# Kernel optimization log

Hardware: AMD Instinct MI355X
Metric: run time of the kernel (lower is better)

## Reference

```python
import jax, jax.numpy as jnp
import numpy as np

NUM_HEADS = 16
EMBED_DIM = 1024
SEQ_LEN = 2048
BATCH = 2


def setup_inputs() -> dict:
    key = jax.random.key(0)
    ks = jax.random.split(key, 7)
    E = EMBED_DIM
    scale = 1.0 / np.sqrt(E)
    return {
        "query": jax.random.normal(ks[0], (SEQ_LEN, BATCH, E), jnp.float32),
        "key": jax.random.normal(ks[1], (SEQ_LEN, BATCH, E), jnp.float32),
        "value": jax.random.normal(ks[2], (SEQ_LEN, BATCH, E), jnp.float32),
        "in_proj_weight": jax.random.normal(ks[3], (3 * E, E), jnp.float32) * scale,
        "in_proj_bias": jnp.zeros((3 * E,), jnp.float32),
        "out_proj_weight": jax.random.normal(ks[4], (E, E), jnp.float32) * scale,
        "out_proj_bias": jnp.zeros((E,), jnp.float32),
    }


def reference(query, key, value, in_proj_weight, in_proj_bias, out_proj_weight, out_proj_bias):
    T, B, E = query.shape
    H = NUM_HEADS
    d = E // H
    scaling = float(d) ** -0.5
    # in-projections: rows [0:E) -> q, [E:2E) -> k, [2E:3E) -> v
    q = query @ in_proj_weight[:E].T + in_proj_bias[:E]
    k = key @ in_proj_weight[E:2 * E].T + in_proj_bias[E:2 * E]
    v = value @ in_proj_weight[2 * E:].T + in_proj_bias[2 * E:]
    q = q * scaling
    # (T, B, E) -> (B*H, T, d)
    q = q.reshape(T, B * H, d).transpose(1, 0, 2)
    k = k.reshape(T, B * H, d).transpose(1, 0, 2)
    v = v.reshape(T, B * H, d).transpose(1, 0, 2)
    S = k.shape[1]
    scores = jnp.einsum('ntd,nsd->nts', q, k)  # (B*H, T, S)
    attn = jax.nn.softmax(scores, axis=-1)
    out = jnp.einsum('nts,nsd->ntd', attn, v)  # (B*H, T, d)
    out = out.transpose(1, 0, 2).reshape(T, B, E)
    out = out @ out_proj_weight.T + out_proj_bias
    attn_avg = attn.reshape(B, H, T, S).sum(axis=1) / H
    return out, attn_avg
```

## Files before the change

kernel.cpp:

```cpp
#include <hip/hip_runtime.h>
#include <math.h>

#define T_LEN 2048
#define BATCH 2
#define EMB 1024
#define NHEAD 16
#define HDIM 64
#define BH (BATCH*NHEAD)
#define MROWS (T_LEN*BATCH)
#define QSCALE (0.125f * 1.4426950408889634f)
#define HEADBUF ((size_t)BH*T_LEN*HDIM)

typedef __attribute__((ext_vector_type(8))) short bf16x8;
typedef __attribute__((ext_vector_type(4))) float f32x4;

#define MFMA16(a,b,c) __builtin_amdgcn_mfma_f32_16x16x32_bf16(a,b,c,0,0,0)

__device__ __forceinline__ short f2bf(float f) {
    union { float f; unsigned u; } v; v.f = f;
    unsigned r = (v.u + 0x7FFFu + ((v.u >> 16) & 1u)) >> 16;
    return (short)(unsigned short)r;
}
__device__ __forceinline__ float bf2f(short s) {
    union { unsigned u; float f; } v; v.u = ((unsigned)(unsigned short)s) << 16;
    return v.f;
}
__device__ __forceinline__ unsigned cvtpk(float a, float b) {
    unsigned r;
    asm("v_cvt_pk_bf16_f32 %0, %1, %2" : "=v"(r) : "v"(a), "v"(b));
    return r;
}
__device__ __forceinline__ void gload16(const void* g, void* l) {
    __builtin_amdgcn_global_load_lds(
        (const __attribute__((address_space(1))) unsigned*)g,
        (__attribute__((address_space(3))) unsigned*)l, 16, 0, 0);
}

__global__ __launch_bounds__(256) void tobf16_kernel(
    const float* __restrict__ q, const float* __restrict__ k,
    const float* __restrict__ v, const float* __restrict__ w,
    const float* __restrict__ wo, short* __restrict__ out)
{
    size_t i8 = ((size_t)blockIdx.x * 256 + threadIdx.x) * 8;
    const float* src; size_t off;
    if (i8 < 12582912) {
        int sel = (int)(i8 >> 22);
        src = (sel == 0) ? q : (sel == 1) ? k : v;
        off = i8 & 4194303;
    } else if (i8 < 15728640) {
        src = w;  off = i8 - 12582912;
    } else {
        src = wo; off = i8 - 15728640;
    }
    float4 f0 = *(const float4*)(src + off);
    float4 f1 = *(const float4*)(src + off + 4);
    bf16x8 o;
    o[0]=f2bf(f0.x); o[1]=f2bf(f0.y); o[2]=f2bf(f0.z); o[3]=f2bf(f0.w);
    o[4]=f2bf(f1.x); o[5]=f2bf(f1.y); o[6]=f2bf(f1.z); o[7]=f2bf(f1.w);
    *(bf16x8*)(out + i8) = o;
}

__global__ __launch_bounds__(256) void inproj_gemm(
    const short* __restrict__ Xq, const short* __restrict__ Xk,
    const short* __restrict__ Xv, const short* __restrict__ Wb,
    const float* __restrict__ bias,
    short* __restrict__ qbuf, short* __restrict__ kbuf, short* __restrict__ vbufT)
{
    const int mBase = blockIdx.x * 128;
    const int nBase = blockIdx.y * 128;
    const int which = nBase >> 10;
    const short* __restrict__ X = (which == 0) ? Xq : (which == 1) ? Xk : Xv;

    __shared__ short Ast[2][128][32];
    __shared__ short Bst[2][128][32];

    const int tid  = threadIdx.x;
    const int lane = tid & 63;
    const int w    = tid >> 6;
    const int wr   = w >> 1, wc = w & 1;
    const int lr   = lane & 15, lg = lane >> 4;

    const int srow = lane >> 2;
    const int schk = (lane & 3) ^ ((lane >> 3) & 3);
    const int fchk = (lg ^ ((lr >> 1) & 3)) * 16;

    f32x4 acc[4][4] = {};

    #pragma unroll
    for (int j = 0; j < 2; ++j) {
        int r = j * 64 + w * 16 + srow;
        gload16(X  + (size_t)(mBase + r) * EMB + schk * 8,
                (char*)Ast[0] + j * 4096 + w * 1024);
        gload16(Wb + (size_t)(nBase + r) * EMB + schk * 8,
                (char*)Bst[0] + j * 4096 + w * 1024);
    }
    __syncthreads();

    int cur = 0;
    for (int kb = 0; kb < EMB; kb += 32) {
        if (kb + 32 < EMB) {
            #pragma unroll
            for (int j = 0; j < 2; ++j) {
                int r = j * 64 + w * 16 + srow;
                gload16(X  + (size_t)(mBase + r) * EMB + kb + 32 + schk * 8,
                        (char*)Ast[cur ^ 1] + j * 4096 + w * 1024);
                gload16(Wb + (size_t)(nBase + r) * EMB + kb + 32 + schk * 8,
                        (char*)Bst[cur ^ 1] + j * 4096 + w * 1024);
            }
        }
        bf16x8 af[4], bfr[4];
        #pragma unroll
        for (int rg = 0; rg < 4; ++rg)
            af[rg] = *(const bf16x8*)((char*)Ast[cur] + (wr * 64 + rg * 16 + lr) * 64 + fchk);
        #pragma unroll
        for (int cg = 0; cg < 4; ++cg)
            bfr[cg] = *(const bf16x8*)((char*)Bst[cur] + (wc * 64 + cg * 16 + lr) * 64 + fchk);
        #pragma unroll
        for (int rg = 0; rg < 4; ++rg)
            #pragma unroll
            for (int cg = 0; cg < 4; ++cg)
                acc[rg][cg] = MFMA16(af[rg], bfr[cg], acc[rg][cg]);
        __syncthreads();
        cur ^= 1;
    }

    #pragma unroll
    for (int rg = 0; rg < 4; ++rg) {
        #pragma unroll
        for (int cg = 0; cg < 4; ++cg) {
            int n  = nBase + wc * 64 + cg * 16 + lr;
            int e  = n & 1023;
            int h  = e >> 6, dd = e & 63;
            float bs = bias[n];
            #pragma unroll
            for (int ri = 0; ri < 4; ++ri) {
                int m = mBase + wr * 64 + rg * 16 + lg * 4 + ri;
                int t = m >> 1, b = m & 1;
                float val = acc[rg][cg][ri] + bs;
                short bfv;
                if (which == 0) { bfv = f2bf(val * QSCALE);
                    qbuf[((size_t)(b * NHEAD + h) * T_LEN + t) * HDIM + dd] = bfv; }
                else if (which == 1) { bfv = f2bf(val);
                    kbuf[((size_t)(b * NHEAD + h) * T_LEN + t) * HDIM + dd] = bfv; }
                else {
                    bfv = f2bf(val);
                    int s5 = t & 31;
                    int kk = ((s5 >> 2) & 3) * 8 + ((s5 >> 4) << 2) + (s5 & 3);
                    int tt = (t & ~31) | kk;
                    vbufT[((size_t)(b * NHEAD + h) * HDIM + dd) * T_LEN + tt] = bfv;
                }
            }
        }
    }
}

__global__ __launch_bounds__(256) void flash_kernel(
    const short* __restrict__ qb, const short* __restrict__ kbuf,
    const short* __restrict__ vbufT, short* __restrict__ h1,
    float* __restrict__ mlws)
{
    const int qt = blockIdx.x;
    const int hb = blockIdx.y;

    __shared__ short Kst[2][64][64];
    __shared__ short Vst[2][64][64];

    const int tid  = threadIdx.x;
    const int lane = tid & 63;
    const int w    = tid >> 6;
    const int lr   = lane & 15, lg = lane >> 4;

    bf16x8 qa0, qa1;
    {
        const short* qsrc = qb + ((size_t)hb * T_LEN + qt * 64 + w * 16 + lr) * HDIM;
        qa0 = *(const bf16x8*)(qsrc + lg * 8);
        qa1 = *(const bf16x8*)(qsrc + 32 + lg * 8);
    }

    const short* kbase = kbuf  + (size_t)hb * T_LEN * HDIM;
    const short* vbase = vbufT + (size_t)hb * HDIM * T_LEN;

    const int krow = lane >> 3;
    const int kc16 = (lane & 7) ^ krow;
    const int rb0 = ((0 + lg) ^ (lr & 7)) * 16;
    const int rb1 = ((4 + lg) ^ (lr & 7)) * 16;

    float l_r = 0.f;
    f32x4 o_acc[4] = {};

    for (int st = 0; st < T_LEN / 128; ++st) {
        __syncthreads();
        #pragma unroll
        for (int it = 0; it < 2; ++it) {
            int r = (w * 2 + it) * 8 + krow;
            #pragma unroll
            for (int sh = 0; sh < 2; ++sh) {
                gload16(kbase + (size_t)(st * 128 + sh * 64 + r) * HDIM + kc16 * 8,
                        (char*)Kst[sh] + (w * 2 + it) * 1024);
                gload16(vbase + (size_t)r * T_LEN + st * 128 + sh * 64 + kc16 * 8,
                        (char*)Vst[sh] + (w * 2 + it) * 1024);
            }
        }
        __syncthreads();

        #pragma unroll
        for (int sh = 0; sh < 2; ++sh) {
            f32x4 sc[4] = {};
            #pragma unroll
            for (int sg = 0; sg < 4; ++sg) {
                const char* krowp = (const char*)Kst[sh] + (sg * 16 + lr) * 128;
                bf16x8 kf0 = *(const bf16x8*)(krowp + rb0);
                bf16x8 kf1 = *(const bf16x8*)(krowp + rb1);
                sc[sg] = MFMA16(kf0, qa0, sc[sg]);
                sc[sg] = MFMA16(kf1, qa1, sc[sg]);
            }

            float p[4][4];
            #pragma unroll
            for (int sg = 0; sg < 4; ++sg)
                #pragma unroll
                for (int ri = 0; ri < 4; ++ri) {
                    p[sg][ri] = exp2f(sc[sg][ri]);
                    l_r += p[sg][ri];
                }

            #pragma unroll
            for (int ks = 0; ks < 2; ++ks) {
                union { unsigned u[4]; bf16x8 v; } pau;
                pau.u[0] = cvtpk(p[ks * 2][0],     p[ks * 2][1]);
                pau.u[1] = cvtpk(p[ks * 2][2],     p[ks * 2][3]);
                pau.u[2] = cvtpk(p[ks * 2 + 1][0], p[ks * 2 + 1][1]);
                pau.u[3] = cvtpk(p[ks * 2 + 1][2], p[ks * 2 + 1][3]);
                #pragma unroll
                for (int dsub = 0; dsub < 4; ++dsub) {
                    const char* vrowp = (const char*)Vst[sh] + (dsub * 16 + lr) * 128;
                    bf16x8 vf = *(const bf16x8*)(vrowp + (ks ? rb1 : rb0));
                    o_acc[dsub] = MFMA16(pau.v, vf, o_acc[dsub]);
                }
            }
        }
    }

    float lsum = l_r;
    lsum += __shfl_xor(lsum, 16);
    lsum += __shfl_xor(lsum, 32);
    float inv = 1.0f / lsum;
    float invq[4];
    #pragma unroll
    for (int ri = 0; ri < 4; ++ri) invq[ri] = __shfl(inv, lg * 20 + ri);
    #pragma unroll
    for (int ri = 0; ri < 4; ++ri) {
        int row = qt * 64 + w * 16 + lg * 4 + ri;
        #pragma unroll
        for (int dsub = 0; dsub < 4; ++dsub) {
            float x = o_acc[dsub][ri] * invq[ri];
            h1[((size_t)hb * T_LEN + row) * HDIM + dsub * 16 + lr] = f2bf(x);
        }
    }
    if (lg == 0) {
        int row = qt * 64 + w * 16 + lr;
        mlws[(size_t)hb * T_LEN + row] = __log2f(lsum);
    }
}

__global__ __launch_bounds__(256) void avg_kernel(
    const short* __restrict__ qbuf, const short* __restrict__ kbuf,
    const float* __restrict__ mlws, float* __restrict__ attn_avg)
{
    const int st = blockIdx.x;
    const int qt = blockIdx.y;
    const int b  = blockIdx.z;

    __shared__ short K2[2][2][64][64];

    const int tid  = threadIdx.x;
    const int lane = tid & 63;
    const int w    = tid >> 6;
    const int lr   = lane & 15, lg = lane >> 4;

    const int krow = lane >> 3;
    const int kc16 = (lane & 7) ^ krow;
    const int rb0 = ((0 + lg) ^ (lr & 7)) * 16;
    const int rb1 = ((4 + lg) ^ (lr & 7)) * 16;

    f32x4 acc[4] = {};

    #pragma unroll
    for (int hh = 0; hh < 2; ++hh) {
        #pragma unroll
        for (int it = 0; it < 2; ++it) {
            int r = (w * 2 + it) * 8 + krow;
            gload16(kbuf + ((size_t)(b * NHEAD + hh) * T_LEN + st * 64 + r) * HDIM + kc16 * 8,
                    (char*)K2[0][hh] + (w * 2 + it) * 1024);
        }
    }
    __syncthreads();

    int cur = 0;
    for (int rnd = 0; rnd < 8; ++rnd) {
        if (rnd + 1 < 8) {
            #pragma unroll
            for (int hh = 0; hh < 2; ++hh) {
                int hbn = b * NHEAD + (rnd + 1) * 2 + hh;
                #pragma unroll
                for (int it = 0; it < 2; ++it) {
                    int r = (w * 2 + it) * 8 + krow;
                    gload16(kbuf + ((size_t)hbn * T_LEN + st * 64 + r) * HDIM + kc16 * 8,
                            (char*)K2[cur ^ 1][hh] + (w * 2 + it) * 1024);
                }
            }
        }
        #pragma unroll
        for (int hh = 0; hh < 2; ++hh) {
            int hb = b * NHEAD + rnd * 2 + hh;
            const short* qsrc = qbuf + ((size_t)hb * T_LEN + qt * 64 + w * 16 + lr) * HDIM;
            bf16x8 qa0 = *(const bf16x8*)(qsrc + lg * 8);
            bf16x8 qa1 = *(const bf16x8*)(qsrc + 32 + lg * 8);

            f32x4 sc[4] = {};
            __builtin_amdgcn_s_setprio(1);
            #pragma unroll
            for (int sg = 0; sg < 4; ++sg) {
                const char* krowp = (const char*)K2[cur][hh] + (sg * 16 + lr) * 128;
                bf16x8 kf0 = *(const bf16x8*)(krowp + rb0);
                bf16x8 kf1 = *(const bf16x8*)(krowp + rb1);
                sc[sg] = MFMA16(qa0, kf0, sc[sg]);
                sc[sg] = MFMA16(qa1, kf1, sc[sg]);
            }
            __builtin_amdgcn_s_setprio(0);

            #pragma unroll
            for (int ri = 0; ri < 4; ++ri) {
                int row = qt * 64 + w * 16 + lg * 4 + ri;
                float ml = mlws[(size_t)hb * T_LEN + row];
                #pragma unroll
                for (int sg = 0; sg < 4; ++sg)
                    acc[sg][ri] += exp2f(sc[sg][ri] - ml);
            }
        }
        __syncthreads();
        cur ^= 1;
    }

    const float invH = 1.0f / (float)NHEAD;
    #pragma unroll
    for (int ri = 0; ri < 4; ++ri) {
        int row = qt * 64 + w * 16 + lg * 4 + ri;
        #pragma unroll
        for (int sg = 0; sg < 4; ++sg)
            attn_avg[((size_t)b * T_LEN + row) * T_LEN + st * 64 + sg * 16 + lr] =
                acc[sg][ri] * invH;
    }
}

__global__ __launch_bounds__(256) void outproj_gemm(
    const short* __restrict__ h1, const short* __restrict__ Wob,
    const float* __restrict__ bo, float* __restrict__ out)
{
    const int mBase = blockIdx.x * 128;
    const int nBase = blockIdx.y * 128;

    __shared__ short Ast[2][128][32];
    __shared__ short Bst[2][128][32];

    const int tid  = threadIdx.x;
    const int lane = tid & 63;
    const int w    = tid >> 6;
    const int wr   = w >> 1, wc = w & 1;
    const int lr   = lane & 15, lg = lane >> 4;

    const int srow = lane >> 2;
    const int schk = (lane & 3) ^ ((lane >> 3) & 3);
    const int fchk = (lg ^ ((lr >> 1) & 3)) * 16;

    f32x4 acc[4][4] = {};

    #define ASRC(r, kb)                                                       \
        (h1 + ((size_t)(((mBase + (r)) & 1) * NHEAD + ((kb) >> 6)) * T_LEN +  \
               ((mBase + (r)) >> 1)) * HDIM + ((kb) & 63) + schk * 8)

    #pragma unroll
    for (int j = 0; j < 2; ++j) {
        int r = j * 64 + w * 16 + srow;
        gload16(ASRC(r, 0), (char*)Ast[0] + j * 4096 + w * 1024);
        gload16(Wob + (size_t)(nBase + r) * EMB + schk * 8,
                (char*)Bst[0] + j * 4096 + w * 1024);
    }
    __syncthreads();

    int cur = 0;
    for (int kb = 0; kb < EMB; kb += 32) {
        if (kb + 32 < EMB) {
            #pragma unroll
            for (int j = 0; j < 2; ++j) {
                int r = j * 64 + w * 16 + srow;
                gload16(ASRC(r, kb + 32), (char*)Ast[cur ^ 1] + j * 4096 + w * 1024);
                gload16(Wob + (size_t)(nBase + r) * EMB + kb + 32 + schk * 8,
                        (char*)Bst[cur ^ 1] + j * 4096 + w * 1024);
            }
        }
        bf16x8 af[4], bfr[4];
        #pragma unroll
        for (int rg = 0; rg < 4; ++rg)
            af[rg] = *(const bf16x8*)((char*)Ast[cur] + (wr * 64 + rg * 16 + lr) * 64 + fchk);
        #pragma unroll
        for (int cg = 0; cg < 4; ++cg)
            bfr[cg] = *(const bf16x8*)((char*)Bst[cur] + (wc * 64 + cg * 16 + lr) * 64 + fchk);
        #pragma unroll
        for (int rg = 0; rg < 4; ++rg)
            #pragma unroll
            for (int cg = 0; cg < 4; ++cg)
                acc[rg][cg] = MFMA16(af[rg], bfr[cg], acc[rg][cg]);
        __syncthreads();
        cur ^= 1;
    }
    #undef ASRC

    #pragma unroll
    for (int rg = 0; rg < 4; ++rg) {
        #pragma unroll
        for (int cg = 0; cg < 4; ++cg) {
            int n = nBase + wc * 64 + cg * 16 + lr;
            float bs = bo[n];
            #pragma unroll
            for (int ri = 0; ri < 4; ++ri) {
                int m = mBase + wr * 64 + rg * 16 + lg * 4 + ri;
                out[(size_t)m * EMB + n] = acc[rg][cg][ri] + bs;
            }
        }
    }
}

extern "C" void kernel_launch(void* const* d_in, const int* in_sizes, int n_in,
                              void* d_out, int out_size, void* d_ws, size_t ws_size,
                              hipStream_t stream)
{
    const float* query = (const float*)d_in[0];
    const float* key   = (const float*)d_in[1];
    const float* value = (const float*)d_in[2];
    const float* ipw   = (const float*)d_in[3];
    const float* ipb   = (const float*)d_in[4];
    const float* opw   = (const float*)d_in[5];
    const float* opb   = (const float*)d_in[6];

    short* qb  = (short*)d_ws;
    short* kb  = qb + HEADBUF;
    short* vbT = kb + HEADBUF;
    short* h1  = vbT + HEADBUF;
    short* h2  = h1 + HEADBUF;
    short* xvb = h2 + HEADBUF;
    short* wbf = xvb + HEADBUF;
    short* wob = wbf + (size_t)3 * EMB * EMB;
    float* mlws = (float*)(wob + (size_t)EMB * EMB);

    float* out      = (float*)d_out;
    float* attn_avg = out + (size_t)MROWS * EMB;

    tobf16_kernel<<<8192, 256, 0, stream>>>(query, key, value, ipw, opw, h1);
    inproj_gemm  <<<dim3(MROWS / 128, 3 * EMB / 128), 256, 0, stream>>>(
        h1, h2, xvb, wbf, ipb, qb, kb, vbT);
    flash_kernel <<<dim3(T_LEN / 64, BH),             256, 0, stream>>>(
        qb, kb, vbT, h1, mlws);
    avg_kernel   <<<dim3(T_LEN / 64, T_LEN / 64, BATCH), 256, 0, stream>>>(
        qb, kb, mlws, attn_avg);
    outproj_gemm <<<dim3(MROWS / 128, EMB / 128),     256, 0, stream>>>(
        h1, wob, opb, out);
}
```

Baseline: 196.6 us.

## Split flash attention over key halves and add a merge kernel

The flash kernel now splits the key/value sequence into two halves along a new grid dimension, doubling the block count from 1024 to 2048. Each half writes unnormalized fp32 partial outputs and row sums, and a new merge kernel adds them, normalizes, converts to bf16 and writes the log-sum. This works without max tracking because the kernel already uses a fixed offset, so the partial sums add directly. The partials are staged in the attn_avg output region before avg_kernel overwrites it, which costs extra global traffic (about 32MB of fp32 partials) and one more kernel launch in exchange for more parallelism.

Result: slower. 201.8 us (+2.6%).

```diff
diff --git a/kernel.cpp b/kernel.cpp
--- a/kernel.cpp
+++ b/kernel.cpp
@@ -156,11 +156,12 @@
 
 __global__ __launch_bounds__(256) void flash_kernel(
     const short* __restrict__ qb, const short* __restrict__ kbuf,
-    const short* __restrict__ vbufT, short* __restrict__ h1,
-    float* __restrict__ mlws)
-{
-    const int qt = blockIdx.x;
-    const int hb = blockIdx.y;
+    const short* __restrict__ vbufT, float* __restrict__ opart,
+    float* __restrict__ lpart)
+{
+    const int qt   = blockIdx.x;
+    const int hb   = blockIdx.y;
+    const int half = blockIdx.z;
 
     __shared__ short Kst[2][64][64];
     __shared__ short Vst[2][64][64];
@@ -179,6 +180,7 @@
 
     const short* kbase = kbuf  + (size_t)hb * T_LEN * HDIM;
     const short* vbase = vbufT + (size_t)hb * HDIM * T_LEN;
+    const int sBase = half * (T_LEN / 2);
 
     const int krow = lane >> 3;
     const int kc16 = (lane & 7) ^ krow;
@@ -188,16 +190,16 @@
     float l_r = 0.f;
     f32x4 o_acc[4] = {};
 
-    for (int st = 0; st < T_LEN / 128; ++st) {
+    for (int st = 0; st < T_LEN / 256; ++st) {
         __syncthreads();
         #pragma unroll
         for (int it = 0; it < 2; ++it) {
             int r = (w * 2 + it) * 8 + krow;
             #pragma unroll
             for (int sh = 0; sh < 2; ++sh) {
-                gload16(kbase + (size_t)(st * 128 + sh * 64 + r) * HDIM + kc16 * 8,
+                gload16(kbase + (size_t)(sBase + st * 128 + sh * 64 + r) * HDIM + kc16 * 8,
                         (char*)Kst[sh] + (w * 2 + it) * 1024);
-                gload16(vbase + (size_t)r * T_LEN + st * 128 + sh * 64 + kc16 * 8,
+                gload16(vbase + (size_t)r * T_LEN + sBase + st * 128 + sh * 64 + kc16 * 8,
                         (char*)Vst[sh] + (w * 2 + it) * 1024);
             }
         }
@@ -244,23 +246,42 @@
     float lsum = l_r;
     lsum += __shfl_xor(lsum, 16);
     lsum += __shfl_xor(lsum, 32);
-    float inv = 1.0f / lsum;
-    float invq[4];
-    #pragma unroll
-    for (int ri = 0; ri < 4; ++ri) invq[ri] = __shfl(inv, lg * 20 + ri);
     #pragma unroll
     for (int ri = 0; ri < 4; ++ri) {
         int row = qt * 64 + w * 16 + lg * 4 + ri;
         #pragma unroll
-        for (int dsub = 0; dsub < 4; ++dsub) {
-            float x = o_acc[dsub][ri] * invq[ri];
-            h1[((size_t)hb * T_LEN + row) * HDIM + dsub * 16 + lr] = f2bf(x);
-        }
+        for (int dsub = 0; dsub < 4; ++dsub)
+            opart[(size_t)half * HEADBUF +
+                  ((size_t)hb * T_LEN + row) * HDIM + dsub * 16 + lr] = o_acc[dsub][ri];
     }
     if (lg == 0) {
         int row = qt * 64 + w * 16 + lr;
-        mlws[(size_t)hb * T_LEN + row] = __log2f(lsum);
-    }
+        lpart[(size_t)half * (BH * T_LEN) + (size_t)hb * T_LEN + row] = lsum;
+    }
+}
+
+__global__ __launch_bounds__(256) void merge_kernel(
+    const float* __restrict__ opart, const float* __restrict__ lpart,
+    short* __restrict__ h1, float* __restrict__ mlws)
+{
+    size_t g = (size_t)blockIdx.x * 256 + threadIdx.x;
+    size_t rowid = g >> 3;
+    int d0 = (int)(g & 7) * 8;
+    float l0 = lpart[rowid];
+    float l1 = lpart[(size_t)BH * T_LEN + rowid];
+    float lsum = l0 + l1;
+    float inv = 1.0f / lsum;
+    const float* p0 = opart + rowid * HDIM + d0;
+    const float* p1 = opart + HEADBUF + rowid * HDIM + d0;
+    float4 a0 = *(const float4*)p0, a1 = *(const float4*)(p0 + 4);
+    float4 b0 = *(const float4*)p1, b1 = *(const float4*)(p1 + 4);
+    bf16x8 o;
+    o[0] = f2bf((a0.x + b0.x) * inv); o[1] = f2bf((a0.y + b0.y) * inv);
+    o[2] = f2bf((a0.z + b0.z) * inv); o[3] = f2bf((a0.w + b0.w) * inv);
+    o[4] = f2bf((a1.x + b1.x) * inv); o[5] = f2bf((a1.y + b1.y) * inv);
+    o[6] = f2bf((a1.z + b1.z) * inv); o[7] = f2bf((a1.w + b1.w) * inv);
+    *(bf16x8*)(h1 + rowid * HDIM + d0) = o;
+    if ((g & 7) == 0) mlws[rowid] = __log2f(lsum);
 }
 
 __global__ __launch_bounds__(256) void avg_kernel(
@@ -451,16 +472,20 @@
     short* xvb = h2 + HEADBUF;
     short* wbf = xvb + HEADBUF;
     short* wob = wbf + (size_t)3 * EMB * EMB;
-    float* mlws = (float*)(wob + (size_t)EMB * EMB);
+    float* mlws  = (float*)(wob + (size_t)EMB * EMB);
+    float* lpart = mlws + (size_t)BH * T_LEN;
 
     float* out      = (float*)d_out;
     float* attn_avg = out + (size_t)MROWS * EMB;
+    float* opart = attn_avg;
 
     tobf16_kernel<<<8192, 256, 0, stream>>>(query, key, value, ipw, opw, h1);
     inproj_gemm  <<<dim3(MROWS / 128, 3 * EMB / 128), 256, 0, stream>>>(
         h1, h2, xvb, wbf, ipb, qb, kb, vbT);
-    flash_kernel <<<dim3(T_LEN / 64, BH),             256, 0, stream>>>(
-        qb, kb, vbT, h1, mlws);
+    flash_kernel <<<dim3(T_LEN / 64, BH, 2),          256, 0, stream>>>(
+        qb, kb, vbT, opart, lpart);
+    merge_kernel <<<2048,                             256, 0, stream>>>(
+        opart, lpart, h1, mlws);
     avg_kernel   <<<dim3(T_LEN / 64, T_LEN / 64, BATCH), 256, 0, stream>>>(
         qb, kb, mlws, attn_avg);
     outproj_gemm <<<dim3(MROWS / 128, EMB / 128),     256, 0, stream>>>(
```
